# Performance work log

Hardware: AMD Instinct MI355X
Metric: run time of the kernel (lower is better)

The kernel has to match this reference:

```python
import jax, jax.numpy as jnp
import numpy as np

CROP_RATE = 0.6
REORDER_RATE = 0.6
MASK_RATE = 0.3
B, L, D = 4096, 200, 64


def setup_inputs() -> dict:
    key = jax.random.key(0)
    k1, k2, k3 = jax.random.split(key, 3)
    seq_input = jax.random.normal(k1, (B, L, D), dtype=jnp.float32)
    seq_len = jax.random.randint(k2, (B,), 1, L + 1).astype(jnp.int32)
    mask_emb = jax.random.normal(k3, (D,), dtype=jnp.float32)
    return {"seq_input": seq_input, "seq_len": seq_len, "mask_emb": mask_emb}


def _augment_one(seq, slen, mask_emb, key):
    """Augment one padded sequence. seq: [L, D], slen: scalar int32.
    Randomly applies one of {crop, reorder, mask} (CL4SRec-style)."""
    L_ = seq.shape[0]
    k_type, k_crop, k_reo_start, k_reo_perm, k_mask = jax.random.split(key, 5)
    pos = jnp.arange(L_)
    valid = pos < slen

    aug_type = jax.random.randint(k_type, (), 0, 3)

    # ---- crop: keep a random contiguous window of length ceil-ish floor(rate*len)
    crop_len = jnp.maximum(1, (CROP_RATE * slen).astype(jnp.int32))
    start_c = jax.random.randint(k_crop, (), 0, jnp.maximum(slen - crop_len, 0) + 1)
    idx_c = jnp.clip(pos + start_c, 0, L_ - 1)
    crop_seq = jnp.where((pos < crop_len)[:, None], seq[idx_c], 0.0)

    # ---- reorder: shuffle a random contiguous window of length floor(rate*len)
    re_len = jnp.maximum(1, (REORDER_RATE * slen).astype(jnp.int32))
    start_r = jax.random.randint(k_reo_start, (), 0, jnp.maximum(slen - re_len, 0) + 1)
    in_win = (pos >= start_r) & (pos < start_r + re_len)
    rand = jax.random.uniform(k_reo_perm, (L_,))
    # window entries get sort-key in [0,1) (random order); others keep position order
    sortkey = jnp.where(in_win, rand, 2.0 + pos.astype(jnp.float32))
    order = jnp.argsort(sortkey)  # first re_len entries: shuffled window indices
    gather_idx = jnp.where(in_win, order[jnp.clip(pos - start_r, 0, L_ - 1)], pos)
    reorder_seq = jnp.where(valid[:, None], seq[gather_idx], 0.0)

    # ---- mask: replace each valid item with mask_emb with prob MASK_RATE
    do_mask = (jax.random.uniform(k_mask, (L_,)) < MASK_RATE) & valid
    mask_seq = jnp.where(do_mask[:, None], mask_emb[None, :], seq)
    mask_seq = jnp.where(valid[:, None], mask_seq, 0.0)

    out = jnp.where(aug_type == 0, crop_seq,
                    jnp.where(aug_type == 1, reorder_seq, mask_seq))
    out_len = jnp.where(aug_type == 0, crop_len, slen).astype(jnp.int32)
    return out, out_len


def reference(seq_input, seq_len, mask_emb):
    keys = jax.random.split(jax.random.key(42), seq_input.shape[0])
    aug_seq, aug_len = jax.vmap(_augment_one, in_axes=(0, 0, None, 0))(
        seq_input, seq_len, mask_emb, keys)
    return aug_seq, aug_len
```

## Files before the change

### kernel.cpp

```cpp
#include <hip/hip_runtime.h>
#include <stdint.h>

#define MAXL 256

__device__ __forceinline__ uint32_t rotl32(uint32_t x, uint32_t d){
  return (x << d) | (x >> (32u - d));
}

__device__ __forceinline__ void tf2x32(uint32_t k0, uint32_t k1,
                                       uint32_t x0, uint32_t x1,
                                       uint32_t& o0, uint32_t& o1){
  const uint32_t k2 = k0 ^ k1 ^ 0x1BD11BDAu;
  x0 += k0; x1 += k1;
  x0 += x1; x1 = rotl32(x1,13); x1 ^= x0;
  x0 += x1; x1 = rotl32(x1,15); x1 ^= x0;
  x0 += x1; x1 = rotl32(x1,26); x1 ^= x0;
  x0 += x1; x1 = rotl32(x1, 6); x1 ^= x0;
  x0 += k1; x1 += k2 + 1u;
  x0 += x1; x1 = rotl32(x1,17); x1 ^= x0;
  x0 += x1; x1 = rotl32(x1,29); x1 ^= x0;
  x0 += x1; x1 = rotl32(x1,16); x1 ^= x0;
  x0 += x1; x1 = rotl32(x1,24); x1 ^= x0;
  x0 += k2; x1 += k0 + 2u;
  x0 += x1; x1 = rotl32(x1,13); x1 ^= x0;
  x0 += x1; x1 = rotl32(x1,15); x1 ^= x0;
  x0 += x1; x1 = rotl32(x1,26); x1 ^= x0;
  x0 += x1; x1 = rotl32(x1, 6); x1 ^= x0;
  x0 += k0; x1 += k1 + 3u;
  x0 += x1; x1 = rotl32(x1,17); x1 ^= x0;
  x0 += x1; x1 = rotl32(x1,29); x1 ^= x0;
  x0 += x1; x1 = rotl32(x1,16); x1 ^= x0;
  x0 += x1; x1 = rotl32(x1,24); x1 ^= x0;
  x0 += k1; x1 += k2 + 4u;
  x0 += x1; x1 = rotl32(x1,13); x1 ^= x0;
  x0 += x1; x1 = rotl32(x1,15); x1 ^= x0;
  x0 += x1; x1 = rotl32(x1,26); x1 ^= x0;
  x0 += x1; x1 = rotl32(x1, 6); x1 ^= x0;
  x0 += k2; x1 += k0 + 5u;
  o0 = x0; o1 = x1;
}

__device__ __forceinline__ float u01(uint32_t bits){
  return __uint_as_float((bits >> 9) | 0x3F800000u) - 1.0f;
}

__device__ __forceinline__ uint32_t randint_comb(uint32_t hb, uint32_t lb, uint32_t span){
  uint32_t mult = 65536u % span;
  mult = (mult * mult) % span;
  return ((hb % span) * mult + (lb % span)) % span;
}

__global__ __launch_bounds__(256)
void seqaug_kernel(const float* __restrict__ seq, const int* __restrict__ slen_arr,
                   const float* __restrict__ memb, float* __restrict__ out,
                   int B, int L, int D)
{
  const int b   = blockIdx.x;
  const int tid = threadIdx.x;

  __shared__ int    s_params[4];
  __shared__ float  s_rand[MAXL];
  __shared__ int    s_src[MAXL];
  __shared__ float4 s_memb[64];

  const int slen = slen_arr[b];
  const int f_per_row = D >> 2;

  uint32_t kb0, kb1;
  tf2x32(0u, 42u, 0u, (uint32_t)b, kb0, kb1);

  int mflag = 0;
  if (tid < L){
    uint32_t a0,a1,c0,c1,r0,r1,m0,m1;
    tf2x32(kb0, kb1, 0u, 3u, a0, a1);
    tf2x32(kb0, kb1, 0u, 4u, c0, c1);
    tf2x32(a0, a1, 0u, (uint32_t)tid, r0, r1);
    tf2x32(c0, c1, 0u, (uint32_t)tid, m0, m1);
    s_rand[tid] = u01(r0 ^ r1);
    mflag = (u01(m0 ^ m1) < 0.3f) ? 1 : 0;
  }
  if (tid >= 224 && tid < 224 + f_per_row)
    s_memb[tid - 224] = ((const float4*)memb)[tid - 224];

  if (tid < 64){
    uint32_t param = (uint32_t)(tid >> 1);
    uint32_t j     = (uint32_t)(tid & 1);
    uint32_t w0,w1,s0,s1,r0,r1;
    tf2x32(kb0, kb1, 0u, param, w0, w1);
    tf2x32(w0, w1, 0u, j, s0, s1);
    tf2x32(s0, s1, 0u, 0u, r0, r1);
    uint32_t bits = r0 ^ r1;
    uint32_t hb_a = __shfl(bits, 0), lb_a = __shfl(bits, 1);
    uint32_t hb_c = __shfl(bits, 2), lb_c = __shfl(bits, 3);
    uint32_t hb_r = __shfl(bits, 4), lb_r = __shfl(bits, 5);
    if (tid == 0){
      int aug_type = (int)randint_comb(hb_a, lb_a, 3u);
      int crop_len = (int)(0.6f * (float)slen);
      if (crop_len < 1) crop_len = 1;
      int span = slen - crop_len; if (span < 0) span = 0;
      int start_c = (int)randint_comb(hb_c, lb_c, (uint32_t)(span + 1));
      int start_r = (int)randint_comb(hb_r, lb_r, (uint32_t)(span + 1));
      s_params[0] = aug_type; s_params[1] = crop_len;
      s_params[2] = start_c;  s_params[3] = start_r;
    }
  }
  __syncthreads();

  const int aug_type = s_params[0];
  const int crop_len = s_params[1];
  const int start_c  = s_params[2];
  const int start_r  = s_params[3];
  const int re_len   = crop_len;

  if (tid < L){
    int p = tid;
    if (aug_type == 0){
      s_src[p] = (p < crop_len) ? (p + start_c) : -1;
    } else if (aug_type == 1){
      bool inwin = (p >= start_r) && (p < start_r + re_len);
      if (!inwin) s_src[p] = (p < slen) ? p : -1;
    } else {
      s_src[p] = (p >= slen) ? -1 : (mflag ? -2 : p);
    }
  }
  if (aug_type == 1 && tid < re_len){
    float kt = s_rand[start_r + tid];
    int rank = 0;
    for (int s = 0; s < re_len; ++s){
      float ks = s_rand[start_r + s];
      rank += (int)((ks < kt) || (ks == kt && s < tid));
    }
    s_src[start_r + rank] = start_r + tid;
  }
  __syncthreads();

  const float4* seq4 = (const float4*)(seq + (size_t)b * L * D);
  float4*       out4 = (float4*)(out + (size_t)b * L * D);
  const float4 zero4 = make_float4(0.f, 0.f, 0.f, 0.f);
  if (f_per_row == 16){
    const int f = tid & 15;
    for (int p = tid >> 4; p < L; p += 16){
      int src = s_src[p];
      float4 v;
      if (src >= 0)       v = seq4[src * 16 + f];
      else if (src == -2) v = s_memb[f];
      else                v = zero4;
      out4[p * 16 + f] = v;
    }
  } else {
    const int total = L * f_per_row;
    for (int idx = tid; idx < total; idx += blockDim.x){
      int p = idx / f_per_row;
      int f = idx - p * f_per_row;
      int src = s_src[p];
      float4 v;
      if (src >= 0)       v = seq4[src * f_per_row + f];
      else if (src == -2) v = s_memb[f];
      else                v = zero4;
      out4[idx] = v;
    }
  }
  if (tid == 0){
    out[(size_t)B * L * D + b] = (float)((aug_type == 0) ? crop_len : slen);
  }
}

extern "C" void kernel_launch(void* const* d_in, const int* in_sizes, int n_in,
                              void* d_out, int out_size, void* d_ws, size_t ws_size,
                              hipStream_t stream) {
  const float* seq  = (const float*)d_in[0];
  const int*   slen = (const int*)  d_in[1];
  const float* memb = (const float*)d_in[2];
  float*       out  = (float*)d_out;
  const int B = in_sizes[1];
  const int D = in_sizes[2];
  const int L = in_sizes[0] / (B * D);
  hipLaunchKernelGGL(seqaug_kernel, dim3(B), dim3(256), 0, stream,
                     seq, slen, memb, out, B, L, D);
}
```

Before: 62.63 us.

## Split augmentation into index-computation kernel and flat gather kernel

The fused per-sequence kernel is split in two. A params kernel computes per-row source indices into workspace, plus the output length. A separate flat, fully parallel gather kernel then copies rows using nontemporal stores. This aims to decouple the RNG and rank work from the bandwidth-bound copy and improve memory-level parallelism. The cost is an extra launch and a round trip of the index array through global memory.

```diff
diff --git a/kernel.cpp b/kernel.cpp
--- a/kernel.cpp
+++ b/kernel.cpp
@@ -2,6 +2,8 @@
 #include <stdint.h>
 
 #define MAXL 256
+
+typedef float f4 __attribute__((ext_vector_type(4)));
 
 __device__ __forceinline__ uint32_t rotl32(uint32_t x, uint32_t d){
   return (x << d) | (x >> (32u - d));
@@ -51,9 +53,8 @@
 }
 
 __global__ __launch_bounds__(256)
-void seqaug_kernel(const float* __restrict__ seq, const int* __restrict__ slen_arr,
-                   const float* __restrict__ memb, float* __restrict__ out,
-                   int B, int L, int D)
+void params_kernel(const int* __restrict__ slen_arr, int* __restrict__ d_src,
+                   float* __restrict__ out_tail, int B, int L)
 {
   const int b   = blockIdx.x;
   const int tid = threadIdx.x;
@@ -61,10 +62,8 @@
   __shared__ int    s_params[4];
   __shared__ float  s_rand[MAXL];
   __shared__ int    s_src[MAXL];
-  __shared__ float4 s_memb[64];
 
   const int slen = slen_arr[b];
-  const int f_per_row = D >> 2;
 
   uint32_t kb0, kb1;
   tf2x32(0u, 42u, 0u, (uint32_t)b, kb0, kb1);
@@ -79,8 +78,6 @@
     s_rand[tid] = u01(r0 ^ r1);
     mflag = (u01(m0 ^ m1) < 0.3f) ? 1 : 0;
   }
-  if (tid >= 224 && tid < 224 + f_per_row)
-    s_memb[tid - 224] = ((const float4*)memb)[tid - 224];
 
   if (tid < 64){
     uint32_t param = (uint32_t)(tid >> 1);
@@ -102,6 +99,7 @@
       int start_r = (int)randint_comb(hb_r, lb_r, (uint32_t)(span + 1));
       s_params[0] = aug_type; s_params[1] = crop_len;
       s_params[2] = start_c;  s_params[3] = start_r;
+      out_tail[b] = (float)((aug_type == 0) ? crop_len : slen);
     }
   }
   __syncthreads();
@@ -134,35 +132,42 @@
   }
   __syncthreads();
 
-  const float4* seq4 = (const float4*)(seq + (size_t)b * L * D);
-  float4*       out4 = (float4*)(out + (size_t)b * L * D);
-  const float4 zero4 = make_float4(0.f, 0.f, 0.f, 0.f);
-  if (f_per_row == 16){
-    const int f = tid & 15;
-    for (int p = tid >> 4; p < L; p += 16){
-      int src = s_src[p];
-      float4 v;
-      if (src >= 0)       v = seq4[src * 16 + f];
-      else if (src == -2) v = s_memb[f];
-      else                v = zero4;
-      out4[p * 16 + f] = v;
-    }
-  } else {
-    const int total = L * f_per_row;
-    for (int idx = tid; idx < total; idx += blockDim.x){
-      int p = idx / f_per_row;
-      int f = idx - p * f_per_row;
-      int src = s_src[p];
-      float4 v;
-      if (src >= 0)       v = seq4[src * f_per_row + f];
-      else if (src == -2) v = s_memb[f];
-      else                v = zero4;
-      out4[idx] = v;
-    }
-  }
-  if (tid == 0){
-    out[(size_t)B * L * D + b] = (float)((aug_type == 0) ? crop_len : slen);
-  }
+  if (tid < L){
+    int s = s_src[tid];
+    d_src[b * L + tid] = (s >= 0) ? (b * L + s) : s;
+  }
+}
+
+__global__ __launch_bounds__(256)
+void scatter_kernel_d64(const f4* __restrict__ seq4, const f4* __restrict__ memb4,
+                        const int* __restrict__ d_src, f4* __restrict__ out4,
+                        int n_rows)
+{
+  const int t   = blockIdx.x * 256 + threadIdx.x;
+  const int row = t >> 4;
+  const int f   = t & 15;
+  if (row >= n_rows) return;
+  const int src = d_src[row];
+  f4 v = {0.f, 0.f, 0.f, 0.f};
+  if (src >= 0)       v = seq4[src * 16 + f];
+  else if (src == -2) v = memb4[f];
+  __builtin_nontemporal_store(v, &out4[(size_t)row * 16 + f]);
+}
+
+__global__ __launch_bounds__(256)
+void scatter_kernel_gen(const f4* __restrict__ seq4, const f4* __restrict__ memb4,
+                        const int* __restrict__ d_src, f4* __restrict__ out4,
+                        int n_rows, int f_per_row)
+{
+  const int t = blockIdx.x * 256 + threadIdx.x;
+  const int row = t / f_per_row;
+  const int f   = t - row * f_per_row;
+  if (row >= n_rows) return;
+  const int src = d_src[row];
+  f4 v = {0.f, 0.f, 0.f, 0.f};
+  if (src >= 0)       v = seq4[src * f_per_row + f];
+  else if (src == -2) v = memb4[f];
+  __builtin_nontemporal_store(v, &out4[(size_t)row * f_per_row + f]);
 }
 
 extern "C" void kernel_launch(void* const* d_in, const int* in_sizes, int n_in,
@@ -175,6 +180,21 @@
   const int B = in_sizes[1];
   const int D = in_sizes[2];
   const int L = in_sizes[0] / (B * D);
-  hipLaunchKernelGGL(seqaug_kernel, dim3(B), dim3(256), 0, stream,
-                     seq, slen, memb, out, B, L, D);
-}
+
+  int* d_src = (int*)d_ws;
+
+  hipLaunchKernelGGL(params_kernel, dim3(B), dim3(256), 0, stream,
+                     slen, d_src, out + (size_t)B * L * D, B, L);
+
+  const int n_rows = B * L;
+  const int fpr = D >> 2;
+  const long total4 = (long)n_rows * fpr;
+  const int grid = (int)((total4 + 255) / 256);
+  if (fpr == 16){
+    hipLaunchKernelGGL(scatter_kernel_d64, dim3(grid), dim3(256), 0, stream,
+                       (const f4*)seq, (const f4*)memb, d_src, (f4*)out, n_rows);
+  } else {
+    hipLaunchKernelGGL(scatter_kernel_gen, dim3(grid), dim3(256), 0, stream,
+                       (const f4*)seq, (const f4*)memb, d_src, (f4*)out, n_rows, fpr);
+  }
+}
```

Result: no change. 61.73 us (-1.4%).

## Generate random keys only for the chosen augmentation and use nontemporal copies

Applied to the files above, without the earlier changes.

Threefry draws for the reorder keys and mask flags are now computed only in the branch matching the chosen augmentation type, instead of computing both for every position. Reorder draws are limited to the window, which adds one extra barrier on that path. The copy loop now uses nontemporal loads and stores with a flat index stride, and the length output is written by the thread that computes the parameters. This reduces the per-block ALU prologue on a memory-bound copy, and nontemporal hints may or may not help caching.

```diff
diff --git a/kernel.cpp b/kernel.cpp
--- a/kernel.cpp
+++ b/kernel.cpp
@@ -2,6 +2,8 @@
 #include <stdint.h>
 
 #define MAXL 256
+
+typedef float f4 __attribute__((ext_vector_type(4)));
 
 __device__ __forceinline__ uint32_t rotl32(uint32_t x, uint32_t d){
   return (x << d) | (x >> (32u - d));
@@ -51,36 +53,26 @@
 }
 
 __global__ __launch_bounds__(256)
-void seqaug_kernel(const float* __restrict__ seq, const int* __restrict__ slen_arr,
-                   const float* __restrict__ memb, float* __restrict__ out,
-                   int B, int L, int D)
+void seqaug_fused(const float* __restrict__ seq, const int* __restrict__ slen_arr,
+                  const float* __restrict__ memb, float* __restrict__ out,
+                  int B, int L, int D)
 {
   const int b   = blockIdx.x;
   const int tid = threadIdx.x;
 
-  __shared__ int    s_params[4];
-  __shared__ float  s_rand[MAXL];
-  __shared__ int    s_src[MAXL];
-  __shared__ float4 s_memb[64];
+  __shared__ int   s_params[4];
+  __shared__ float s_rand[MAXL];
+  __shared__ int   s_src[MAXL];
+  __shared__ f4    s_memb[64];
 
   const int slen = slen_arr[b];
-  const int f_per_row = D >> 2;
+  const int fpr  = D >> 2;
 
   uint32_t kb0, kb1;
   tf2x32(0u, 42u, 0u, (uint32_t)b, kb0, kb1);
 
-  int mflag = 0;
-  if (tid < L){
-    uint32_t a0,a1,c0,c1,r0,r1,m0,m1;
-    tf2x32(kb0, kb1, 0u, 3u, a0, a1);
-    tf2x32(kb0, kb1, 0u, 4u, c0, c1);
-    tf2x32(a0, a1, 0u, (uint32_t)tid, r0, r1);
-    tf2x32(c0, c1, 0u, (uint32_t)tid, m0, m1);
-    s_rand[tid] = u01(r0 ^ r1);
-    mflag = (u01(m0 ^ m1) < 0.3f) ? 1 : 0;
-  }
-  if (tid >= 224 && tid < 224 + f_per_row)
-    s_memb[tid - 224] = ((const float4*)memb)[tid - 224];
+  if (tid >= 64 && tid < 64 + fpr)
+    s_memb[tid - 64] = ((const f4*)memb)[tid - 64];
 
   if (tid < 64){
     uint32_t param = (uint32_t)(tid >> 1);
@@ -102,6 +94,7 @@
       int start_r = (int)randint_comb(hb_r, lb_r, (uint32_t)(span + 1));
       s_params[0] = aug_type; s_params[1] = crop_len;
       s_params[2] = start_c;  s_params[3] = start_r;
+      out[(size_t)B * L * D + b] = (float)((aug_type == 0) ? crop_len : slen);
     }
   }
   __syncthreads();
@@ -110,58 +103,70 @@
   const int crop_len = s_params[1];
   const int start_c  = s_params[2];
   const int start_r  = s_params[3];
-  const int re_len   = crop_len;
 
-  if (tid < L){
-    int p = tid;
-    if (aug_type == 0){
-      s_src[p] = (p < crop_len) ? (p + start_c) : -1;
-    } else if (aug_type == 1){
-      bool inwin = (p >= start_r) && (p < start_r + re_len);
-      if (!inwin) s_src[p] = (p < slen) ? p : -1;
-    } else {
-      s_src[p] = (p >= slen) ? -1 : (mflag ? -2 : p);
+  if (aug_type == 0){
+    if (tid < L)
+      s_src[tid] = (tid < crop_len) ? (tid + start_c) : -1;
+  } else if (aug_type == 2){
+    if (tid < L){
+      uint32_t c0,c1,m0,m1;
+      tf2x32(kb0, kb1, 0u, 4u, c0, c1);
+      tf2x32(c0, c1, 0u, (uint32_t)tid, m0, m1);
+      int mflag = (u01(m0 ^ m1) < 0.3f) ? 1 : 0;
+      s_src[tid] = (tid >= slen) ? -1 : (mflag ? -2 : tid);
     }
-  }
-  if (aug_type == 1 && tid < re_len){
-    float kt = s_rand[start_r + tid];
-    int rank = 0;
-    for (int s = 0; s < re_len; ++s){
-      float ks = s_rand[start_r + s];
-      rank += (int)((ks < kt) || (ks == kt && s < tid));
+  } else {
+    const int re_len = crop_len;
+    if (tid < re_len){
+      uint32_t a0,a1,r0,r1;
+      tf2x32(kb0, kb1, 0u, 3u, a0, a1);
+      tf2x32(a0, a1, 0u, (uint32_t)(start_r + tid), r0, r1);
+      s_rand[tid] = u01(r0 ^ r1);
     }
-    s_src[start_r + rank] = start_r + tid;
+    if (tid < L){
+      bool inwin = (tid >= start_r) && (tid < start_r + re_len);
+      if (!inwin) s_src[tid] = (tid < slen) ? tid : -1;
+    }
+    __syncthreads();
+    if (tid < re_len){
+      float kt = s_rand[tid];
+      int rank = 0;
+      for (int s = 0; s < re_len; ++s){
+        float ks = s_rand[s];
+        rank += (int)((ks < kt) || (ks == kt && s < tid));
+      }
+      s_src[start_r + rank] = start_r + tid;
+    }
   }
   __syncthreads();
 
-  const float4* seq4 = (const float4*)(seq + (size_t)b * L * D);
-  float4*       out4 = (float4*)(out + (size_t)b * L * D);
-  const float4 zero4 = make_float4(0.f, 0.f, 0.f, 0.f);
-  if (f_per_row == 16){
-    const int f = tid & 15;
-    for (int p = tid >> 4; p < L; p += 16){
-      int src = s_src[p];
-      float4 v;
-      if (src >= 0)       v = seq4[src * 16 + f];
+  const f4* seq4 = (const f4*)(seq + (size_t)b * L * D);
+  f4*       out4 = (f4*)(out + (size_t)b * L * D);
+  const f4 zero4 = {0.f, 0.f, 0.f, 0.f};
+  if (fpr == 16){
+    const int total = L * 16;
+    for (int idx = tid; idx < total; idx += 256){
+      const int p = idx >> 4;
+      const int f = idx & 15;
+      const int src = s_src[p];
+      f4 v;
+      if (src >= 0)       v = __builtin_nontemporal_load(&seq4[src * 16 + f]);
       else if (src == -2) v = s_memb[f];
       else                v = zero4;
-      out4[p * 16 + f] = v;
+      __builtin_nontemporal_store(v, &out4[idx]);
     }
   } else {
-    const int total = L * f_per_row;
-    for (int idx = tid; idx < total; idx += blockDim.x){
-      int p = idx / f_per_row;
-      int f = idx - p * f_per_row;
-      int src = s_src[p];
-      float4 v;
-      if (src >= 0)       v = seq4[src * f_per_row + f];
+    const int total = L * fpr;
+    for (int idx = tid; idx < total; idx += 256){
+      const int p = idx / fpr;
+      const int f = idx - p * fpr;
+      const int src = s_src[p];
+      f4 v;
+      if (src >= 0)       v = __builtin_nontemporal_load(&seq4[src * fpr + f]);
       else if (src == -2) v = s_memb[f];
       else                v = zero4;
-      out4[idx] = v;
+      __builtin_nontemporal_store(v, &out4[idx]);
     }
-  }
-  if (tid == 0){
-    out[(size_t)B * L * D + b] = (float)((aug_type == 0) ? crop_len : slen);
   }
 }
 
@@ -175,6 +180,7 @@
   const int B = in_sizes[1];
   const int D = in_sizes[2];
   const int L = in_sizes[0] / (B * D);
-  hipLaunchKernelGGL(seqaug_kernel, dim3(B), dim3(256), 0, stream,
+
+  hipLaunchKernelGGL(seqaug_fused, dim3(B), dim3(256), 0, stream,
                      seq, slen, memb, out, B, L, D);
 }
```

After: 66.57 us. +6.3%, slower.
